# Kernel optimization log

Hardware: AMD Instinct MI355X
Metric: run time of the kernel (lower is better)

Reference implementation:

```python
import jax, jax.numpy as jnp
import numpy as np

N_NODES = 100000
N_EDGES = 1600000
F_NODE = 32
F_EDGE = 32
HID = 64
N_TGT = 32


def setup_inputs() -> dict:
    key = jax.random.key(0)
    ks = jax.random.split(key, 12)
    x = jax.random.normal(ks[0], (N_NODES, F_NODE), dtype=jnp.float32)
    edge_index = jax.random.randint(ks[1], (2, N_EDGES), 0, N_NODES, dtype=jnp.int64)
    edge_attr = jax.random.normal(ks[2], (N_EDGES, F_EDGE), dtype=jnp.float32)
    u = jax.random.normal(ks[3], (1, 8), dtype=jnp.float32)
    batch = jnp.zeros((N_NODES,), dtype=jnp.int64)
    s1 = 1.0 / np.sqrt(F_NODE + F_EDGE)
    s2 = 1.0 / np.sqrt(HID)
    s3 = 1.0 / np.sqrt(HID + F_NODE)
    W1a = jax.random.uniform(ks[4], (F_NODE + F_EDGE, HID), jnp.float32, -s1, s1)
    b1a = jax.random.uniform(ks[5], (HID,), jnp.float32, -s1, s1)
    W1b = jax.random.uniform(ks[6], (HID, HID), jnp.float32, -s2, s2)
    b1b = jax.random.uniform(ks[7], (HID,), jnp.float32, -s2, s2)
    W2a = jax.random.uniform(ks[8], (HID + F_NODE, HID), jnp.float32, -s3, s3)
    b2a = jax.random.uniform(ks[9], (HID,), jnp.float32, -s3, s3)
    W2b = jax.random.uniform(ks[10], (HID, N_TGT), jnp.float32, -s2, s2)
    b2b = jax.random.uniform(ks[11], (N_TGT,), jnp.float32, -s2, s2)
    return {"x": x, "edge_index": edge_index, "edge_attr": edge_attr, "u": u,
            "batch": batch, "W1a": W1a, "b1a": b1a, "W1b": W1b, "b1b": b1b,
            "W2a": W2a, "b2a": b2a, "W2b": W2b, "b2b": b2b}


def reference(x, edge_index, edge_attr, u, batch,
              W1a, b1a, W1b, b1b, W2a, b2a, W2b, b2b):
    row, col = edge_index[0], edge_index[1]
    n = x.shape[0]
    # gather source node features and concat with edge features -> edge MLP
    m = jnp.concatenate([x[col], edge_attr], axis=1)           # [E, F_NODE+F_EDGE]
    m = jax.nn.relu(m @ W1a + b1a) @ W1b + b1b                  # [E, HID]
    # scatter-mean back to destination nodes (row)
    summed = jax.ops.segment_sum(m, row, num_segments=n)        # [N, HID]
    counts = jax.ops.segment_sum(jnp.ones((m.shape[0],), m.dtype), row, num_segments=n)
    agg = summed / jnp.maximum(counts, 1.0)[:, None]
    h = jnp.concatenate([x, agg], axis=1)                       # [N, HID+F_NODE]
    out = jax.nn.relu(h @ W2a + b2a) @ W2b + b2b                # [N, N_TGT]
    return out
```

## Files before the change

kernel.cpp:

```cpp
#include <hip/hip_runtime.h>

#define NN 100000
#define NE 1600000
#define NB ((NN + 255) / 256)

typedef unsigned int uint32;
typedef unsigned short ushort16;
typedef float f32x4 __attribute__((ext_vector_type(4)));
typedef short bf16x8 __attribute__((ext_vector_type(8)));

__device__ __forceinline__ float bflo(uint32 u) { return __uint_as_float(u << 16); }
__device__ __forceinline__ float bfhi(uint32 u) { return __uint_as_float(u & 0xffff0000u); }
__device__ __forceinline__ uint32 bfbits(float v) { return (__float_as_uint(v) + 0x8000u) >> 16; }
__device__ __forceinline__ uint32 pack2(float a, float b) { return bfbits(a) | (bfbits(b) << 16); }

__device__ __forceinline__ int sigma_ch(int c) {
    return (((c >> 2) & 3) << 4) + (((c >> 4) & 3) << 2) + (c & 3);
}

__global__ __launch_bounds__(256) void k_hist_rank(const int* __restrict__ ei, int* __restrict__ deg,
                                                   int* __restrict__ rank, int E) {
    int e = blockIdx.x * 256 + threadIdx.x;
    if (e < E) rank[e] = atomicAdd(&deg[ei[e]], 1);
}

__global__ __launch_bounds__(256) void k_hist(const int* __restrict__ ei, int* __restrict__ deg, int E) {
    int e = blockIdx.x * 256 + threadIdx.x;
    if (e < E) atomicAdd(&deg[ei[e]], 1);
}

__global__ __launch_bounds__(256) void k_scan1(const int* __restrict__ deg, int* __restrict__ offs,
                                               int* __restrict__ bsums, int n) {
    __shared__ int s[256];
    int tid = threadIdx.x;
    int i = blockIdx.x * 256 + tid;
    int v = (i < n) ? deg[i] : 0;
    int acc = v;
    s[tid] = acc;
    __syncthreads();
    #pragma unroll
    for (int off = 1; off < 256; off <<= 1) {
        int t = (tid >= off) ? s[tid - off] : 0;
        __syncthreads();
        acc += t;
        s[tid] = acc;
        __syncthreads();
    }
    if (i < n) offs[i] = acc - v;
    if (tid == 255) bsums[blockIdx.x] = acc;
}

__global__ __launch_bounds__(512) void k_scan2(int* __restrict__ bsums, int nb) {
    __shared__ int s[512];
    int tid = threadIdx.x;
    int v = (tid < nb) ? bsums[tid] : 0;
    int acc = v;
    s[tid] = acc;
    __syncthreads();
    #pragma unroll
    for (int off = 1; off < 512; off <<= 1) {
        int t = (tid >= off) ? s[tid - off] : 0;
        __syncthreads();
        acc += t;
        s[tid] = acc;
        __syncthreads();
    }
    bsums[tid] = acc - v;
}

__global__ __launch_bounds__(256) void k_offs(int* __restrict__ offs, const int* __restrict__ bsums, int n) {
    int i = blockIdx.x * 256 + threadIdx.x;
    if (i < n) offs[i] += bsums[i >> 8];
}

__global__ __launch_bounds__(256) void k_sorted(const int* __restrict__ ei, const int* __restrict__ offs,
                                                const int* __restrict__ rank, int2* __restrict__ ecol, int E) {
    int e = blockIdx.x * 256 + threadIdx.x;
    if (e >= E) return;
    int slot = offs[ei[e]] + rank[e];
    ecol[slot] = make_int2(e, ei[E + e]);
}

__global__ __launch_bounds__(256) void k_prep(const float* __restrict__ W1b, const float* __restrict__ b1b,
                                              const float* __restrict__ W2a, const float* __restrict__ W1a,
                                              float* __restrict__ Wc, float* __restrict__ bc,
                                              uint4* __restrict__ wpack, int perm) {
    int t = blockIdx.x * 256 + threadIdx.x;
    int r = t >> 6, c = t & 63;
    float a = 0.f;
    for (int k = 0; k < 64; ++k) a += W1b[r * 64 + k] * W2a[(32 + k) * 64 + c];
    int rs = perm ? sigma_ch(r) : r;
    Wc[rs * 64 + c] = a;
    if (t < 64) {
        float bacc = 0.f;
        for (int k = 0; k < 64; ++k) bacc += b1b[k] * W2a[(32 + k) * 64 + t];
        bc[t] = bacc;
    }
    if (t < 512) {
        int table = t >> 8;
        int cc = (t >> 6) & 3;
        int lane = t & 63;
        int qq = lane >> 4, en = lane & 15;
        int ch = cc * 16 + en;
        uint32 w[4];
        #pragma unroll
        for (int j = 0; j < 4; ++j) {
            int k0 = qq * 8 + j * 2;
            int row0 = (table ? 0 : 32) + k0;
            w[j] = pack2(W1a[row0 * 64 + ch], W1a[(row0 + 1) * 64 + ch]);
        }
        wpack[t] = make_uint4(w[0], w[1], w[2], w[3]);
    }
}

__global__ __launch_bounds__(256) void k_edge_fused(
    const float* __restrict__ ea, const float* __restrict__ x,
    const uint4* __restrict__ wpack, const float* __restrict__ b1a,
    const int* __restrict__ deg, const int* __restrict__ offs, const int2* __restrict__ ecol,
    float* __restrict__ Sacc)
{
    int lane = threadIdx.x & 63;
    int wave = threadIdx.x >> 6;
    int en = lane & 15;
    int qq = lane >> 4;
    int node = blockIdx.x * 4 + wave;
    if (node >= NN) return;

    union { uint4 u; bf16x8 v; } wB[4], wA[4];
    #pragma unroll
    for (int cc = 0; cc < 4; ++cc) {
        wB[cc].u = wpack[cc * 64 + lane];
        wA[cc].u = wpack[256 + cc * 64 + lane];
    }
    f32x4 binit[4];
    #pragma unroll
    for (int cc = 0; cc < 4; ++cc) {
        float4 b = *(const float4*)(b1a + cc * 16 + qq * 4);
        binit[cc] = (f32x4){b.x, b.y, b.z, b.w};
    }

    int d = deg[node];
    int start = offs[node];

    f32x4 tot[4];
    #pragma unroll
    for (int cc = 0; cc < 4; ++cc) tot[cc] = (f32x4){0.f, 0.f, 0.f, 0.f};

    #pragma unroll 1
    for (int t0 = 0; t0 < d; t0 += 16) {
        int sidx = t0 + en;
        bool ok = sidx < d;
        int slot = start + (ok ? sidx : d - 1);
        int2 ec = ecol[slot];

        const float* ar = ea + (size_t)ec.x * 32 + qq * 8;
        float4 a0 = *(const float4*)ar;
        float4 a1 = *(const float4*)(ar + 4);
        const float* xr = x + (size_t)ec.y * 32 + qq * 8;
        float4 x0 = *(const float4*)xr;
        float4 x1 = *(const float4*)(xr + 4);

        union { uint4 u; bf16x8 v; } bea, bx;
        f32x4 acc[4];
        if (ok) {
            bea.u.x = pack2(a0.x, a0.y); bea.u.y = pack2(a0.z, a0.w);
            bea.u.z = pack2(a1.x, a1.y); bea.u.w = pack2(a1.z, a1.w);
            bx.u.x = pack2(x0.x, x0.y); bx.u.y = pack2(x0.z, x0.w);
            bx.u.z = pack2(x1.x, x1.y); bx.u.w = pack2(x1.z, x1.w);
            #pragma unroll
            for (int cc = 0; cc < 4; ++cc) acc[cc] = binit[cc];
        } else {
            bea.u = make_uint4(0, 0, 0, 0);
            bx.u = make_uint4(0, 0, 0, 0);
            #pragma unroll
            for (int cc = 0; cc < 4; ++cc) acc[cc] = (f32x4){0.f, 0.f, 0.f, 0.f};
        }
        #pragma unroll
        for (int cc = 0; cc < 4; ++cc)
            acc[cc] = __builtin_amdgcn_mfma_f32_16x16x32_bf16(wB[cc].v, bea.v, acc[cc], 0, 0, 0);
        #pragma unroll
        for (int cc = 0; cc < 4; ++cc)
            acc[cc] = __builtin_amdgcn_mfma_f32_16x16x32_bf16(wA[cc].v, bx.v, acc[cc], 0, 0, 0);
        #pragma unroll
        for (int cc = 0; cc < 4; ++cc) {
            #pragma unroll
            for (int r = 0; r < 4; ++r)
                tot[cc][r] += fmaxf(acc[cc][r], 0.f);
        }
    }

    #pragma unroll
    for (int m = 1; m < 16; m <<= 1) {
        #pragma unroll
        for (int cc = 0; cc < 4; ++cc) {
            #pragma unroll
            for (int r = 0; r < 4; ++r)
                tot[cc][r] += __shfl_xor(tot[cc][r], m);
        }
    }
    if (en == 0) {
        float* sp = Sacc + (size_t)node * 64 + qq * 16;
        #pragma unroll
        for (int cc = 0; cc < 4; ++cc)
            *(float4*)(sp + cc * 4) = make_float4(tot[cc][0], tot[cc][1], tot[cc][2], tot[cc][3]);
    }
}

__global__ __launch_bounds__(256) void k_edge_atom(
    const float* __restrict__ x, const int* __restrict__ ei, const float* __restrict__ ea,
    const float* __restrict__ W1a, const float* __restrict__ b1a,
    float* __restrict__ Sacc, int E)
{
    __shared__ float sWB[32 * 64];
    __shared__ float sWA[32 * 64];
    __shared__ float sb[64];
    for (int t = threadIdx.x; t < 32 * 64; t += 256) {
        sWB[t] = W1a[32 * 64 + t];
        sWA[t] = W1a[t];
    }
    if (threadIdx.x < 64) sb[threadIdx.x] = b1a[threadIdx.x];
    __syncthreads();
    int e = blockIdx.x * 256 + threadIdx.x;
    if (e >= E) return;
    int row = ei[e];
    int col = ei[NE + e];
    float h[64];
    #pragma unroll
    for (int j = 0; j < 64; ++j) h[j] = sb[j];
    const float4* xrow = (const float4*)(x + (size_t)col * 32);
    #pragma unroll
    for (int k4 = 0; k4 < 8; ++k4) {
        float4 v = xrow[k4];
        float vv[4] = {v.x, v.y, v.z, v.w};
        #pragma unroll
        for (int c = 0; c < 4; ++c) {
            float val = vv[c];
            const float4* wr = (const float4*)&sWA[(k4 * 4 + c) * 64];
            #pragma unroll
            for (int j4 = 0; j4 < 16; ++j4) {
                float4 w = wr[j4];
                h[j4 * 4 + 0] += val * w.x; h[j4 * 4 + 1] += val * w.y;
                h[j4 * 4 + 2] += val * w.z; h[j4 * 4 + 3] += val * w.w;
            }
        }
    }
    const float4* earow = (const float4*)(ea + (size_t)e * 32);
    #pragma unroll
    for (int k4 = 0; k4 < 8; ++k4) {
        float4 v = earow[k4];
        float vv[4] = {v.x, v.y, v.z, v.w};
        #pragma unroll
        for (int c = 0; c < 4; ++c) {
            float val = vv[c];
            const float4* wr = (const float4*)&sWB[(k4 * 4 + c) * 64];
            #pragma unroll
            for (int j4 = 0; j4 < 16; ++j4) {
                float4 w = wr[j4];
                h[j4 * 4 + 0] += val * w.x; h[j4 * 4 + 1] += val * w.y;
                h[j4 * 4 + 2] += val * w.z; h[j4 * 4 + 3] += val * w.w;
            }
        }
    }
    float* srow = Sacc + (size_t)row * 64;
    #pragma unroll
    for (int j = 0; j < 64; ++j) atomicAdd(&srow[j], fmaxf(h[j], 0.f));
}

__global__ __launch_bounds__(256) void k_node(
    const float* __restrict__ x, const float* __restrict__ Sacc, const int* __restrict__ deg,
    const float* __restrict__ Wc, const float* __restrict__ bc,
    const float* __restrict__ W2a, const float* __restrict__ b2a,
    const float* __restrict__ W2b, const float* __restrict__ b2b,
    float* __restrict__ out, int N)
{
    __shared__ float sWc[64 * 64];
    __shared__ float sW2ax[32 * 64];
    __shared__ float sW2b[64 * 32];
    __shared__ float sbc2[64];
    __shared__ float sb2[64];
    __shared__ float sb2b_[32];
    for (int t = threadIdx.x; t < 64 * 64; t += 256) sWc[t] = Wc[t];
    for (int t = threadIdx.x; t < 32 * 64; t += 256) sW2ax[t] = W2a[t];
    for (int t = threadIdx.x; t < 64 * 32; t += 256) sW2b[t] = W2b[t];
    if (threadIdx.x < 64) {
        sbc2[threadIdx.x] = bc[threadIdx.x] + b2a[threadIdx.x];
        sb2[threadIdx.x] = b2a[threadIdx.x];
    }
    if (threadIdx.x < 32) sb2b_[threadIdx.x] = b2b[threadIdx.x];
    __syncthreads();

    int i = blockIdx.x * 256 + threadIdx.x;
    if (i >= N) return;
    int d = deg[i];
    float inv = (d > 0) ? 1.f / (float)d : 0.f;

    float h2[64];
    #pragma unroll
    for (int j = 0; j < 64; ++j) h2[j] = (d > 0) ? sbc2[j] : sb2[j];

    const float4* sp = (const float4*)(Sacc + (size_t)i * 64);
    #pragma unroll 2
    for (int k4 = 0; k4 < 16; ++k4) {
        float4 v = sp[k4];
        float vv[4] = {v.x * inv, v.y * inv, v.z * inv, v.w * inv};
        #pragma unroll
        for (int c = 0; c < 4; ++c) {
            float val = vv[c];
            const float4* wr = (const float4*)&sWc[(k4 * 4 + c) * 64];
            #pragma unroll
            for (int j4 = 0; j4 < 16; ++j4) {
                float4 w = wr[j4];
                h2[j4 * 4 + 0] += val * w.x; h2[j4 * 4 + 1] += val * w.y;
                h2[j4 * 4 + 2] += val * w.z; h2[j4 * 4 + 3] += val * w.w;
            }
        }
    }
    const float4* xrow = (const float4*)(x + (size_t)i * 32);
    #pragma unroll 2
    for (int k4 = 0; k4 < 8; ++k4) {
        float4 v = xrow[k4];
        float vv[4] = {v.x, v.y, v.z, v.w};
        #pragma unroll
        for (int c = 0; c < 4; ++c) {
            float val = vv[c];
            const float4* wr = (const float4*)&sW2ax[(k4 * 4 + c) * 64];
            #pragma unroll
            for (int j4 = 0; j4 < 16; ++j4) {
                float4 w = wr[j4];
                h2[j4 * 4 + 0] += val * w.x; h2[j4 * 4 + 1] += val * w.y;
                h2[j4 * 4 + 2] += val * w.z; h2[j4 * 4 + 3] += val * w.w;
            }
        }
    }
    #pragma unroll
    for (int j = 0; j < 64; ++j) h2[j] = fmaxf(h2[j], 0.f);

    float o[32];
    #pragma unroll
    for (int j = 0; j < 32; ++j) o[j] = sb2b_[j];
    #pragma unroll
    for (int k = 0; k < 64; ++k) {
        float val = h2[k];
        const float4* wr = (const float4*)&sW2b[k * 32];
        #pragma unroll
        for (int j4 = 0; j4 < 8; ++j4) {
            float4 w = wr[j4];
            o[j4 * 4 + 0] += val * w.x; o[j4 * 4 + 1] += val * w.y;
            o[j4 * 4 + 2] += val * w.z; o[j4 * 4 + 3] += val * w.w;
        }
    }
    float4* orow = (float4*)(out + (size_t)i * 32);
    #pragma unroll
    for (int q = 0; q < 8; ++q)
        orow[q] = make_float4(o[q * 4], o[q * 4 + 1], o[q * 4 + 2], o[q * 4 + 3]);
}

extern "C" void kernel_launch(void* const* d_in, const int* in_sizes, int n_in,
                              void* d_out, int out_size, void* d_ws, size_t ws_size,
                              hipStream_t stream) {
    const float* x   = (const float*)d_in[0];
    const int*   ei  = (const int*)d_in[1];
    const float* ea  = (const float*)d_in[2];
    const float* W1a = (const float*)d_in[5];
    const float* b1a = (const float*)d_in[6];
    const float* W1b = (const float*)d_in[7];
    const float* b1b = (const float*)d_in[8];
    const float* W2a = (const float*)d_in[9];
    const float* b2a = (const float*)d_in[10];
    const float* W2b = (const float*)d_in[11];
    const float* b2b = (const float*)d_in[12];
    float* out = (float*)d_out;

    char* p = (char*)d_ws;
    int* deg        = (int*)p;        p += (size_t)NN * 4;
    int* offs       = (int*)p;        p += (size_t)NN * 4;
    int* bsums      = (int*)p;        p += 2048;
    float* Wc       = (float*)p;      p += 4096 * 4;
    float* bc       = (float*)p;      p += 64 * 4;
    uint4* wpack    = (uint4*)p;      p += 512 * 16;
    size_t off_fb   = (size_t)(p - (char*)d_ws);
    int* rank       = (int*)p;        p += (size_t)NE * 4;
    int2* ecol      = (int2*)p;       p += (size_t)NE * 8;
    float* Sacc     = (float*)p;      p += (size_t)NN * 64 * 4;
    size_t need     = (size_t)(p - (char*)d_ws);

    dim3 blk(256);

    if (ws_size >= need) {
        hipMemsetAsync(deg, 0, (size_t)NN * 4, stream);
        hipLaunchKernelGGL(k_hist_rank, dim3((NE + 255) / 256), blk, 0, stream, ei, deg, rank, NE);
        hipLaunchKernelGGL(k_scan1, dim3(NB), blk, 0, stream, deg, offs, bsums, NN);
        hipLaunchKernelGGL(k_scan2, dim3(1), dim3(512), 0, stream, bsums, NB);
        hipLaunchKernelGGL(k_offs, dim3(NB), blk, 0, stream, offs, bsums, NN);
        hipLaunchKernelGGL(k_sorted, dim3((NE + 255) / 256), blk, 0, stream, ei, offs, rank, ecol, NE);
        hipLaunchKernelGGL(k_prep, dim3(16), blk, 0, stream, W1b, b1b, W2a, W1a, Wc, bc, wpack, 1);
        hipLaunchKernelGGL(k_edge_fused, dim3((NN + 3) / 4), blk, 0, stream,
                           ea, x, wpack, b1a, deg, offs, ecol, Sacc);
        hipLaunchKernelGGL(k_node, dim3(NB), blk, 0, stream,
                           x, Sacc, deg, Wc, bc, W2a, b2a, W2b, b2b, out, NN);
    } else {
        float* Sacc_fb = (float*)((char*)d_ws + off_fb);
        hipMemsetAsync(deg, 0, (size_t)NN * 4, stream);
        hipMemsetAsync(Sacc_fb, 0, (size_t)NN * 64 * 4, stream);
        hipLaunchKernelGGL(k_hist, dim3((NE + 255) / 256), blk, 0, stream, ei, deg, NE);
        hipLaunchKernelGGL(k_prep, dim3(16), blk, 0, stream, W1b, b1b, W2a, W1a, Wc, bc, wpack, 0);
        hipLaunchKernelGGL(k_edge_atom, dim3((NE + 255) / 256), blk, 0, stream,
                           x, ei, ea, W1a, b1a, Sacc_fb, NE);
        hipLaunchKernelGGL(k_node, dim3(NB), blk, 0, stream,
                           x, Sacc_fb, deg, Wc, bc, W2a, b2a, W2b, b2b, out, NN);
    }
}
```

Measured before the change: 313.4 us.

## Process two destination nodes per wave with hoisted first-tile gathers

```diff
diff --git a/kernel.cpp b/kernel.cpp
--- a/kernel.cpp
+++ b/kernel.cpp
@@ -113,6 +113,39 @@
     }
 }
 
+__device__ __forceinline__ void do_tile(
+    const float4& a0, const float4& a1, const float4& x0, const float4& x1, bool ok,
+    const bf16x8* wB, const bf16x8* wA, const f32x4* binit, f32x4* tot)
+{
+    union { uint4 u; bf16x8 v; } bea, bx;
+    f32x4 acc[4];
+    if (ok) {
+        bea.u.x = pack2(a0.x, a0.y); bea.u.y = pack2(a0.z, a0.w);
+        bea.u.z = pack2(a1.x, a1.y); bea.u.w = pack2(a1.z, a1.w);
+        bx.u.x = pack2(x0.x, x0.y); bx.u.y = pack2(x0.z, x0.w);
+        bx.u.z = pack2(x1.x, x1.y); bx.u.w = pack2(x1.z, x1.w);
+        #pragma unroll
+        for (int cc = 0; cc < 4; ++cc) acc[cc] = binit[cc];
+    } else {
+        bea.u = make_uint4(0, 0, 0, 0);
+        bx.u = make_uint4(0, 0, 0, 0);
+        #pragma unroll
+        for (int cc = 0; cc < 4; ++cc) acc[cc] = (f32x4){0.f, 0.f, 0.f, 0.f};
+    }
+    #pragma unroll
+    for (int cc = 0; cc < 4; ++cc)
+        acc[cc] = __builtin_amdgcn_mfma_f32_16x16x32_bf16(wB[cc], bea.v, acc[cc], 0, 0, 0);
+    #pragma unroll
+    for (int cc = 0; cc < 4; ++cc)
+        acc[cc] = __builtin_amdgcn_mfma_f32_16x16x32_bf16(wA[cc], bx.v, acc[cc], 0, 0, 0);
+    #pragma unroll
+    for (int cc = 0; cc < 4; ++cc) {
+        #pragma unroll
+        for (int r = 0; r < 4; ++r)
+            tot[cc][r] += fmaxf(acc[cc][r], 0.f);
+    }
+}
+
 __global__ __launch_bounds__(256) void k_edge_fused(
     const float* __restrict__ ea, const float* __restrict__ x,
     const uint4* __restrict__ wpack, const float* __restrict__ b1a,
@@ -123,15 +156,21 @@
     int wave = threadIdx.x >> 6;
     int en = lane & 15;
     int qq = lane >> 4;
-    int node = blockIdx.x * 4 + wave;
-    if (node >= NN) return;
-
-    union { uint4 u; bf16x8 v; } wB[4], wA[4];
+    int wid = blockIdx.x * 4 + wave;
+    int nA = wid * 2;
+    if (nA >= NN) return;
+    int nB = nA + 1;
+    bool hasB = (nB < NN);
+
+    union U { uint4 u; bf16x8 v; };
+    U wBu[4], wAu[4];
     #pragma unroll
     for (int cc = 0; cc < 4; ++cc) {
-        wB[cc].u = wpack[cc * 64 + lane];
-        wA[cc].u = wpack[256 + cc * 64 + lane];
-    }
+        wBu[cc].u = wpack[cc * 64 + lane];
+        wAu[cc].u = wpack[256 + cc * 64 + lane];
+    }
+    bf16x8 wB[4] = {wBu[0].v, wBu[1].v, wBu[2].v, wBu[3].v};
+    bf16x8 wA[4] = {wAu[0].v, wAu[1].v, wAu[2].v, wAu[3].v};
     f32x4 binit[4];
     #pragma unroll
     for (int cc = 0; cc < 4; ++cc) {
@@ -139,70 +178,92 @@
         binit[cc] = (f32x4){b.x, b.y, b.z, b.w};
     }
 
-    int d = deg[node];
-    int start = offs[node];
-
-    f32x4 tot[4];
-    #pragma unroll
-    for (int cc = 0; cc < 4; ++cc) tot[cc] = (f32x4){0.f, 0.f, 0.f, 0.f};
+    int dA = deg[nA], stA = offs[nA];
+    int dB = hasB ? deg[nB] : 0;
+    int stB = hasB ? offs[nB] : stA;
+
+    int slA = stA + (en < dA ? en : (dA > 0 ? dA - 1 : 0));
+    if (slA > NE - 1) slA = NE - 1;
+    int slB = stB + (en < dB ? en : (dB > 0 ? dB - 1 : 0));
+    if (slB > NE - 1) slB = NE - 1;
+    int2 ecA = ecol[slA];
+    int2 ecB = ecol[slB];
+
+    const float* arA = ea + (size_t)ecA.x * 32 + qq * 8;
+    float4 aA0 = *(const float4*)arA;
+    float4 aA1 = *(const float4*)(arA + 4);
+    const float* xrA = x + (size_t)ecA.y * 32 + qq * 8;
+    float4 xA0 = *(const float4*)xrA;
+    float4 xA1 = *(const float4*)(xrA + 4);
+
+    const float* arB = ea + (size_t)ecB.x * 32 + qq * 8;
+    float4 aB0 = *(const float4*)arB;
+    float4 aB1 = *(const float4*)(arB + 4);
+    const float* xrB = x + (size_t)ecB.y * 32 + qq * 8;
+    float4 xB0 = *(const float4*)xrB;
+    float4 xB1 = *(const float4*)(xrB + 4);
+
+    f32x4 totA[4], totB[4];
+    #pragma unroll
+    for (int cc = 0; cc < 4; ++cc) {
+        totA[cc] = (f32x4){0.f, 0.f, 0.f, 0.f};
+        totB[cc] = (f32x4){0.f, 0.f, 0.f, 0.f};
+    }
+
+    do_tile(aA0, aA1, xA0, xA1, en < dA, wB, wA, binit, totA);
+    do_tile(aB0, aB1, xB0, xB1, en < dB, wB, wA, binit, totB);
 
     #pragma unroll 1
-    for (int t0 = 0; t0 < d; t0 += 16) {
+    for (int t0 = 16; t0 < dA; t0 += 16) {
         int sidx = t0 + en;
-        bool ok = sidx < d;
-        int slot = start + (ok ? sidx : d - 1);
-        int2 ec = ecol[slot];
-
+        bool ok = sidx < dA;
+        int sl = stA + (ok ? sidx : dA - 1);
+        int2 ec = ecol[sl];
         const float* ar = ea + (size_t)ec.x * 32 + qq * 8;
         float4 a0 = *(const float4*)ar;
         float4 a1 = *(const float4*)(ar + 4);
         const float* xr = x + (size_t)ec.y * 32 + qq * 8;
         float4 x0 = *(const float4*)xr;
         float4 x1 = *(const float4*)(xr + 4);
-
-        union { uint4 u; bf16x8 v; } bea, bx;
-        f32x4 acc[4];
-        if (ok) {
-            bea.u.x = pack2(a0.x, a0.y); bea.u.y = pack2(a0.z, a0.w);
-            bea.u.z = pack2(a1.x, a1.y); bea.u.w = pack2(a1.z, a1.w);
-            bx.u.x = pack2(x0.x, x0.y); bx.u.y = pack2(x0.z, x0.w);
-            bx.u.z = pack2(x1.x, x1.y); bx.u.w = pack2(x1.z, x1.w);
-            #pragma unroll
-            for (int cc = 0; cc < 4; ++cc) acc[cc] = binit[cc];
-        } else {
-            bea.u = make_uint4(0, 0, 0, 0);
-            bx.u = make_uint4(0, 0, 0, 0);
-            #pragma unroll
-            for (int cc = 0; cc < 4; ++cc) acc[cc] = (f32x4){0.f, 0.f, 0.f, 0.f};
-        }
+        do_tile(a0, a1, x0, x1, ok, wB, wA, binit, totA);
+    }
+    #pragma unroll 1
+    for (int t0 = 16; t0 < dB; t0 += 16) {
+        int sidx = t0 + en;
+        bool ok = sidx < dB;
+        int sl = stB + (ok ? sidx : dB - 1);
+        int2 ec = ecol[sl];
+        const float* ar = ea + (size_t)ec.x * 32 + qq * 8;
+        float4 a0 = *(const float4*)ar;
+        float4 a1 = *(const float4*)(ar + 4);
+        const float* xr = x + (size_t)ec.y * 32 + qq * 8;
+        float4 x0 = *(const float4*)xr;
+        float4 x1 = *(const float4*)(xr + 4);
+        do_tile(a0, a1, x0, x1, ok, wB, wA, binit, totB);
+    }
+
+    #pragma unroll
+    for (int m = 1; m < 16; m <<= 1) {
+        #pragma unroll
+        for (int cc = 0; cc < 4; ++cc) {
+            #pragma unroll
+            for (int r = 0; r < 4; ++r) {
+                totA[cc][r] += __shfl_xor(totA[cc][r], m);
+                totB[cc][r] += __shfl_xor(totB[cc][r], m);
+            }
+        }
+    }
+    if (en == 0) {
+        float* spA = Sacc + (size_t)nA * 64 + qq * 16;
         #pragma unroll
         for (int cc = 0; cc < 4; ++cc)
-            acc[cc] = __builtin_amdgcn_mfma_f32_16x16x32_bf16(wB[cc].v, bea.v, acc[cc], 0, 0, 0);
-        #pragma unroll
-        for (int cc = 0; cc < 4; ++cc)
-            acc[cc] = __builtin_amdgcn_mfma_f32_16x16x32_bf16(wA[cc].v, bx.v, acc[cc], 0, 0, 0);
-        #pragma unroll
-        for (int cc = 0; cc < 4; ++cc) {
-            #pragma unroll
-            for (int r = 0; r < 4; ++r)
-                tot[cc][r] += fmaxf(acc[cc][r], 0.f);
-        }
-    }
-
-    #pragma unroll
-    for (int m = 1; m < 16; m <<= 1) {
-        #pragma unroll
-        for (int cc = 0; cc < 4; ++cc) {
-            #pragma unroll
-            for (int r = 0; r < 4; ++r)
-                tot[cc][r] += __shfl_xor(tot[cc][r], m);
-        }
-    }
-    if (en == 0) {
-        float* sp = Sacc + (size_t)node * 64 + qq * 16;
-        #pragma unroll
-        for (int cc = 0; cc < 4; ++cc)
-            *(float4*)(sp + cc * 4) = make_float4(tot[cc][0], tot[cc][1], tot[cc][2], tot[cc][3]);
+            *(float4*)(spA + cc * 4) = make_float4(totA[cc][0], totA[cc][1], totA[cc][2], totA[cc][3]);
+        if (hasB) {
+            float* spB = Sacc + (size_t)nB * 64 + qq * 16;
+            #pragma unroll
+            for (int cc = 0; cc < 4; ++cc)
+                *(float4*)(spB + cc * 4) = make_float4(totB[cc][0], totB[cc][1], totB[cc][2], totB[cc][3]);
+        }
     }
 }
 
@@ -394,7 +455,8 @@
         hipLaunchKernelGGL(k_offs, dim3(NB), blk, 0, stream, offs, bsums, NN);
         hipLaunchKernelGGL(k_sorted, dim3((NE + 255) / 256), blk, 0, stream, ei, offs, rank, ecol, NE);
         hipLaunchKernelGGL(k_prep, dim3(16), blk, 0, stream, W1b, b1b, W2a, W1a, Wc, bc, wpack, 1);
-        hipLaunchKernelGGL(k_edge_fused, dim3((NN + 3) / 4), blk, 0, stream,
+        int nwaves = (NN + 1) / 2;
+        hipLaunchKernelGGL(k_edge_fused, dim3((nwaves + 3) / 4), blk, 0, stream,
                            ea, x, wpack, b1a, deg, offs, ecol, Sacc);
         hipLaunchKernelGGL(k_node, dim3(NB), blk, 0, stream,
                            x, Sacc, deg, Wc, bc, W2a, b2a, W2b, b2b, out, NN);
```

Result: no change. 311.5 us (-0.6%).

## Pre-permute edge attributes into sorted bf16 buffer and pre-convert x to bf16

Applied to the files above, without the earlier changes.

```diff
diff --git a/kernel.cpp b/kernel.cpp
--- a/kernel.cpp
+++ b/kernel.cpp
@@ -73,12 +73,35 @@
     if (i < n) offs[i] += bsums[i >> 8];
 }
 
-__global__ __launch_bounds__(256) void k_sorted(const int* __restrict__ ei, const int* __restrict__ offs,
-                                                const int* __restrict__ rank, int2* __restrict__ ecol, int E) {
+__global__ __launch_bounds__(256) void k_scatter_ea(
+    const int* __restrict__ ei, const float* __restrict__ ea,
+    const int* __restrict__ offs, const int* __restrict__ rank,
+    uint32* __restrict__ easw, int* __restrict__ colv)
+{
     int e = blockIdx.x * 256 + threadIdx.x;
-    if (e >= E) return;
-    int slot = offs[ei[e]] + rank[e];
-    ecol[slot] = make_int2(e, ei[E + e]);
+    if (e >= NE) return;
+    int row = ei[e], col = ei[NE + e];
+    int slot = offs[row] + rank[e];
+    const float4* s = (const float4*)(ea + (size_t)e * 32);
+    uint32* dst = easw + (size_t)slot * 16;
+    #pragma unroll
+    for (int q = 0; q < 4; ++q) {
+        float4 v0 = s[q * 2];
+        float4 v1 = s[q * 2 + 1];
+        uint4 o;
+        o.x = pack2(v0.x, v0.y); o.y = pack2(v0.z, v0.w);
+        o.z = pack2(v1.x, v1.y); o.w = pack2(v1.z, v1.w);
+        *(uint4*)(dst + q * 4) = o;
+    }
+    colv[slot] = col;
+}
+
+__global__ __launch_bounds__(256) void k_xb(const float* __restrict__ x, uint32* __restrict__ xbw, int n) {
+    int i = blockIdx.x * 256 + threadIdx.x;
+    if (i < n) {
+        float2 v = *(const float2*)(x + (size_t)2 * i);
+        xbw[i] = pack2(v.x, v.y);
+    }
 }
 
 __global__ __launch_bounds__(256) void k_prep(const float* __restrict__ W1b, const float* __restrict__ b1b,
@@ -114,9 +137,9 @@
 }
 
 __global__ __launch_bounds__(256) void k_edge_fused(
-    const float* __restrict__ ea, const float* __restrict__ x,
+    const uint32* __restrict__ easw, const uint32* __restrict__ xbw, const int* __restrict__ colv,
     const uint4* __restrict__ wpack, const float* __restrict__ b1a,
-    const int* __restrict__ deg, const int* __restrict__ offs, const int2* __restrict__ ecol,
+    const int* __restrict__ deg, const int* __restrict__ offs,
     float* __restrict__ Sacc)
 {
     int lane = threadIdx.x & 63;
@@ -126,7 +149,8 @@
     int node = blockIdx.x * 4 + wave;
     if (node >= NN) return;
 
-    union { uint4 u; bf16x8 v; } wB[4], wA[4];
+    union U { uint4 u; bf16x8 v; };
+    U wB[4], wA[4];
     #pragma unroll
     for (int cc = 0; cc < 4; ++cc) {
         wB[cc].u = wpack[cc * 64 + lane];
@@ -146,46 +170,42 @@
     #pragma unroll
     for (int cc = 0; cc < 4; ++cc) tot[cc] = (f32x4){0.f, 0.f, 0.f, 0.f};
 
-    #pragma unroll 1
-    for (int t0 = 0; t0 < d; t0 += 16) {
-        int sidx = t0 + en;
-        bool ok = sidx < d;
-        int slot = start + (ok ? sidx : d - 1);
-        int2 ec = ecol[slot];
-
-        const float* ar = ea + (size_t)ec.x * 32 + qq * 8;
-        float4 a0 = *(const float4*)ar;
-        float4 a1 = *(const float4*)(ar + 4);
-        const float* xr = x + (size_t)ec.y * 32 + qq * 8;
-        float4 x0 = *(const float4*)xr;
-        float4 x1 = *(const float4*)(xr + 4);
-
-        union { uint4 u; bf16x8 v; } bea, bx;
-        f32x4 acc[4];
-        if (ok) {
-            bea.u.x = pack2(a0.x, a0.y); bea.u.y = pack2(a0.z, a0.w);
-            bea.u.z = pack2(a1.x, a1.y); bea.u.w = pack2(a1.z, a1.w);
-            bx.u.x = pack2(x0.x, x0.y); bx.u.y = pack2(x0.z, x0.w);
-            bx.u.z = pack2(x1.x, x1.y); bx.u.w = pack2(x1.z, x1.w);
-            #pragma unroll
-            for (int cc = 0; cc < 4; ++cc) acc[cc] = binit[cc];
-        } else {
-            bea.u = make_uint4(0, 0, 0, 0);
-            bx.u = make_uint4(0, 0, 0, 0);
-            #pragma unroll
-            for (int cc = 0; cc < 4; ++cc) acc[cc] = (f32x4){0.f, 0.f, 0.f, 0.f};
-        }
-        #pragma unroll
-        for (int cc = 0; cc < 4; ++cc)
-            acc[cc] = __builtin_amdgcn_mfma_f32_16x16x32_bf16(wB[cc].v, bea.v, acc[cc], 0, 0, 0);
-        #pragma unroll
-        for (int cc = 0; cc < 4; ++cc)
-            acc[cc] = __builtin_amdgcn_mfma_f32_16x16x32_bf16(wA[cc].v, bx.v, acc[cc], 0, 0, 0);
-        #pragma unroll
-        for (int cc = 0; cc < 4; ++cc) {
-            #pragma unroll
-            for (int r = 0; r < 4; ++r)
-                tot[cc][r] += fmaxf(acc[cc][r], 0.f);
+    if (d > 0) {
+        #pragma unroll 1
+        for (int t0 = 0; t0 < d; t0 += 16) {
+            int sidx = t0 + en;
+            bool ok = sidx < d;
+            int slot = start + (ok ? sidx : d - 1);
+
+            uint4 beu = *(const uint4*)(easw + (size_t)slot * 16 + qq * 4);
+            int col = colv[slot];
+            uint4 bxu = *(const uint4*)(xbw + (size_t)col * 16 + qq * 4);
+
+            U bea, bx;
+            f32x4 acc[4];
+            if (ok) {
+                bea.u = beu;
+                bx.u = bxu;
+                #pragma unroll
+                for (int cc = 0; cc < 4; ++cc) acc[cc] = binit[cc];
+            } else {
+                bea.u = make_uint4(0, 0, 0, 0);
+                bx.u = make_uint4(0, 0, 0, 0);
+                #pragma unroll
+                for (int cc = 0; cc < 4; ++cc) acc[cc] = (f32x4){0.f, 0.f, 0.f, 0.f};
+            }
+            #pragma unroll
+            for (int cc = 0; cc < 4; ++cc)
+                acc[cc] = __builtin_amdgcn_mfma_f32_16x16x32_bf16(wB[cc].v, bea.v, acc[cc], 0, 0, 0);
+            #pragma unroll
+            for (int cc = 0; cc < 4; ++cc)
+                acc[cc] = __builtin_amdgcn_mfma_f32_16x16x32_bf16(wA[cc].v, bx.v, acc[cc], 0, 0, 0);
+            #pragma unroll
+            for (int cc = 0; cc < 4; ++cc) {
+                #pragma unroll
+                for (int r = 0; r < 4; ++r)
+                    tot[cc][r] += fmaxf(acc[cc][r], 0.f);
+            }
         }
     }
 
@@ -380,7 +400,9 @@
     uint4* wpack    = (uint4*)p;      p += 512 * 16;
     size_t off_fb   = (size_t)(p - (char*)d_ws);
     int* rank       = (int*)p;        p += (size_t)NE * 4;
-    int2* ecol      = (int2*)p;       p += (size_t)NE * 8;
+    int* colv       = (int*)p;        p += (size_t)NE * 4;
+    uint32* xbw     = (uint32*)p;     p += (size_t)NN * 16 * 4;
+    uint32* easw    = (uint32*)p;     p += (size_t)NE * 16 * 4;
     float* Sacc     = (float*)p;      p += (size_t)NN * 64 * 4;
     size_t need     = (size_t)(p - (char*)d_ws);
 
@@ -392,10 +414,12 @@
         hipLaunchKernelGGL(k_scan1, dim3(NB), blk, 0, stream, deg, offs, bsums, NN);
         hipLaunchKernelGGL(k_scan2, dim3(1), dim3(512), 0, stream, bsums, NB);
         hipLaunchKernelGGL(k_offs, dim3(NB), blk, 0, stream, offs, bsums, NN);
-        hipLaunchKernelGGL(k_sorted, dim3((NE + 255) / 256), blk, 0, stream, ei, offs, rank, ecol, NE);
+        hipLaunchKernelGGL(k_scatter_ea, dim3((NE + 255) / 256), blk, 0, stream,
+                           ei, ea, offs, rank, easw, colv);
+        hipLaunchKernelGGL(k_xb, dim3((NN * 16 + 255) / 256), blk, 0, stream, x, xbw, NN * 16);
         hipLaunchKernelGGL(k_prep, dim3(16), blk, 0, stream, W1b, b1b, W2a, W1a, Wc, bc, wpack, 1);
         hipLaunchKernelGGL(k_edge_fused, dim3((NN + 3) / 4), blk, 0, stream,
-                           ea, x, wpack, b1a, deg, offs, ecol, Sacc);
+                           easw, xbw, colv, wpack, b1a, deg, offs, Sacc);
         hipLaunchKernelGGL(k_node, dim3(NB), blk, 0, stream,
                            x, Sacc, deg, Wc, bc, W2a, b2a, W2b, b2b, out, NN);
     } else {
```

Result: slower. 344.6 us (+10.0%).
